# Optimization experiments

Measured on AMD Instinct MI355X. Metric: run time of the kernel, lower is better.

## Reference

```python
import jax, jax.numpy as jnp
import numpy as np

EPS = 1e-5

def conv_block(x, w, b, a, g, bt):
    # x: [B,Cin,T,F]; w: [Cout,Cin]; b: [Cout]; a: scalar PReLU slope; g,bt: [Cout,F]
    y = jnp.einsum('bctf,oc->botf', x, w) + b[None, :, None, None]
    y = jnp.maximum(y, 0.0) + a * jnp.minimum(y, 0.0)  # PReLU (single shared slope)
    mu = jnp.mean(y, axis=(1, 3), keepdims=True)
    var = jnp.var(y, axis=(1, 3), keepdims=True)       # unbiased=False
    y = (y - mu) / jnp.sqrt(var + EPS)
    return y * g[None, :, None, :] + bt[None, :, None, :]

# vmap over heads: weights have leading head axis, x is shared
_head_block = jax.vmap(conv_block, in_axes=(None, 0, 0, 0, 0, 0))


def setup_inputs() -> dict:
    key = jax.random.key(0)
    B, C, T, F = 8, 64, 1024, 64
    H, HID = 4, 4
    DV = C // H
    ks = jax.random.split(key, 16)
    s = 1.0 / np.sqrt(C)
    inp = {
        'x': jax.random.normal(ks[0], (B, C, T, F), jnp.float32),
        # per-head Q conv blocks
        'qw': jax.random.normal(ks[1], (H, HID, C), jnp.float32) * s,
        'qb': jax.random.normal(ks[2], (H, HID), jnp.float32) * 0.01,
        'qa': jnp.full((H,), 0.25, jnp.float32),
        'qg': jnp.ones((H, HID, F), jnp.float32),
        'qbeta': jnp.zeros((H, HID, F), jnp.float32),
        # per-head K conv blocks
        'kw': jax.random.normal(ks[3], (H, HID, C), jnp.float32) * s,
        'kb': jax.random.normal(ks[4], (H, HID), jnp.float32) * 0.01,
        'ka': jnp.full((H,), 0.25, jnp.float32),
        'kg': jnp.ones((H, HID, F), jnp.float32),
        'kbeta': jnp.zeros((H, HID, F), jnp.float32),
        # per-head V conv blocks (out = C//H)
        'vw': jax.random.normal(ks[5], (H, DV, C), jnp.float32) * s,
        'vb': jax.random.normal(ks[6], (H, DV), jnp.float32) * 0.01,
        'va': jnp.full((H,), 0.25, jnp.float32),
        'vg': jnp.ones((H, DV, F), jnp.float32),
        'vbeta': jnp.zeros((H, DV, F), jnp.float32),
        # final 'likear' conv block
        'lw': jax.random.normal(ks[7], (C, C), jnp.float32) * s,
        'lb': jax.random.normal(ks[8], (C,), jnp.float32) * 0.01,
        'la': jnp.float32(0.25),
        'lg': jnp.ones((C, F), jnp.float32),
        'lbeta': jnp.zeros((C, F), jnp.float32),
    }
    return inp


def reference(x, qw, qb, qa, qg, qbeta, kw, kb, ka, kg, kbeta,
              vw, vb, va, vg, vbeta, lw, lb, la, lg, lbeta):
    B, C, T, F = x.shape
    H = qw.shape[0]
    HID = qw.shape[1]
    DV = C // H
    embed = H * F  # embed_size = num_heads * num_freqs

    Q = _head_block(x, qw, qb, qa, qg, qbeta)  # [H,B,HID,T,F]
    K = _head_block(x, kw, kb, ka, kg, kbeta)  # [H,B,HID,T,F]
    V = _head_block(x, vw, vb, va, vg, vbeta)  # [H,B,DV,T,F]

    # cat over dim 0 == head-major reshape; transpose(1,2)+flatten(2)
    Ql = Q.reshape(H * B, HID, T, F).transpose(0, 2, 1, 3).reshape(H * B, T, HID * F)
    Kl = K.reshape(H * B, HID, T, F).transpose(0, 2, 1, 3).reshape(H * B, T, HID * F)
    Vl = V.reshape(H * B, DV, T, F).transpose(0, 2, 1, 3).reshape(H * B, T, DV * F)

    scores = jnp.einsum('ntd,nsd->nts', Ql, Kl) / jnp.sqrt(jnp.float32(embed))
    attn = jax.nn.softmax(scores, axis=-1)               # [HB,T,T]
    A = jnp.einsum('nts,nsd->ntd', attn, Vl)             # [HB,T,DV*F]

    A = A.reshape(H * B, T, DV, F).transpose(0, 2, 1, 3)  # [HB,DV,T,F]
    A = A.reshape(H, B, DV, T, F).transpose(1, 0, 2, 3, 4).reshape(B, C, T, F)

    out = conv_block(A, lw, lb, la, lg, lbeta)
    return out + x
```

## Files before the change

kernel.cpp:

```cpp
#include <hip/hip_runtime.h>

typedef unsigned short u16;
typedef unsigned int u32;
typedef __attribute__((ext_vector_type(8))) short short8;
typedef __attribute__((ext_vector_type(4))) float f32x4;

#define EPSV 1e-5f

__device__ __forceinline__ u16 f2bf(float f) {
    unsigned u = __float_as_uint(f);
    u += 0x7fffu + ((u >> 16) & 1u);
    return (u16)(u >> 16);
}

__device__ __forceinline__ f32x4 mfma_bf16(short8 a, short8 b, f32x4 c) {
    return __builtin_amdgcn_mfma_f32_16x16x32_bf16(a, b, c, 0, 0, 0);
}

__device__ __forceinline__ void gload_lds16(const void* g, void* l) {
    __builtin_amdgcn_global_load_lds((const __attribute__((address_space(1))) void*)g,
                                     (__attribute__((address_space(3))) void*)l, 16, 0, 0);
}

__device__ __forceinline__ u32 packgb(float g, float bt) {
    return (u32)f2bf(g) | ((u32)f2bf(bt) << 16);
}

__global__ __launch_bounds__(256) void k_prep_qkv(
    const float* __restrict__ qw, const float* __restrict__ kw, const float* __restrict__ vw,
    u16* __restrict__ wq)
{
    const int tid = threadIdx.x;
#pragma unroll
    for (int i = 0; i < 24; i++) {
        int idx = tid + i * 256;
        int row = idx >> 6;
        float wv = (row < 16) ? qw[idx] : ((row < 32) ? kw[idx - 1024] : vw[idx - 2048]);
        wq[idx] = f2bf(wv);
    }
}

__global__ __launch_bounds__(256) void k_prep_l(
    const float* __restrict__ lw, const float* __restrict__ lg, const float* __restrict__ lbt,
    u16* __restrict__ lwb, u32* __restrict__ lgb)
{
    const int tid = threadIdx.x;
#pragma unroll
    for (int i = 0; i < 16; i++) {
        int idx = tid + i * 256;
        lwb[idx] = f2bf(lw[idx]);
        lgb[idx] = packgb(lg[idx], lbt[idx]);
    }
}

__global__ __launch_bounds__(512) void k_qkv(
    const float* __restrict__ x, const u16* __restrict__ wq,
    const float* __restrict__ qb, const float* __restrict__ qa,
    const float* __restrict__ qg, const float* __restrict__ qbt,
    const float* __restrict__ kb, const float* __restrict__ ka,
    const float* __restrict__ kg, const float* __restrict__ kbt,
    const float* __restrict__ vb, const float* __restrict__ va,
    const float* __restrict__ vg, const float* __restrict__ vbt,
    u16* __restrict__ Qb, u16* __restrict__ Kb, u16* __restrict__ Vb)
{
    __shared__ u16 xT[64][66];
    __shared__ float ys[96][66];
    __shared__ float bias_s[96], slope_s[96];

    const int tid = threadIdx.x, w = tid >> 6, lane = tid & 63;
    const int b = blockIdx.x >> 10, t = blockIdx.x & 1023;
    const int lc = lane & 15, grp = lane >> 4;

    if (tid < 96) {
        int row = tid; float bv, sv;
        if (row < 16)      { bv = qb[row];      sv = qa[row >> 2]; }
        else if (row < 32) { bv = kb[row - 16]; sv = ka[(row - 16) >> 2]; }
        else               { bv = vb[row - 32]; sv = va[(row - 32) >> 4]; }
        bias_s[row] = bv; slope_s[row] = sv;
    }
    const float* xbt = x + ((size_t)(b * 64) * 1024 + t) * 64;
#pragma unroll
    for (int k = 0; k < 2; k++) {
        int chunk = tid + k * 512;
        int c = chunk >> 4, q = chunk & 15;
        float4 v = *(const float4*)(xbt + (size_t)c * 65536 + q * 4);
        xT[q * 4 + 0][c] = f2bf(v.x);
        xT[q * 4 + 1][c] = f2bf(v.y);
        xT[q * 4 + 2][c] = f2bf(v.z);
        xT[q * 4 + 3][c] = f2bf(v.w);
    }
    __syncthreads();

#pragma unroll
    for (int i = 0; i < 3; i++) {
        int tile = w * 3 + i;
        int mt = tile >> 2, nt = tile & 3;
        f32x4 acc = {0.f, 0.f, 0.f, 0.f};
#pragma unroll
        for (int kt = 0; kt < 2; kt++) {
            short8 a  = *(const short8*)(wq + (mt * 16 + lc) * 64 + kt * 32 + grp * 8);
            short8 bf = *(const short8*)(&xT[nt * 16 + lc][kt * 32 + grp * 8]);
            acc = mfma_bf16(a, bf, acc);
        }
        int colf = nt * 16 + lc;
#pragma unroll
        for (int j = 0; j < 4; j++) {
            int row = mt * 16 + grp * 4 + j;
            float y = acc[j] + bias_s[row];
            float sl = slope_s[row];
            y = (y > 0.f) ? y : sl * y;
            ys[row][colf] = y;
        }
    }
    __syncthreads();

    if (w < 4) {
        const int h = w;
        float v0[16]; float s = 0.f, ss = 0.f;
#pragma unroll
        for (int o = 0; o < 16; o++) { float y = ys[32 + h * 16 + o][lane]; v0[o] = y; s += y; ss += y * y; }
#pragma unroll
        for (int m = 1; m < 64; m <<= 1) { s += __shfl_xor(s, m, 64); ss += __shfl_xor(ss, m, 64); }
        float mu = s * (1.f / 1024.f), var = ss * (1.f / 1024.f) - mu * mu;
        float rs = rsqrtf(var + EPSV);
        size_t base = ((size_t)(h * 8 + b) * 1024 + t) * 1024;
#pragma unroll
        for (int o = 0; o < 16; o++) {
            float val = (v0[o] - mu) * rs * vg[(h * 16 + o) * 64 + lane] + vbt[(h * 16 + o) * 64 + lane];
            Vb[base + o * 64 + lane] = f2bf(val);
        }
    } else {
        const int h = w - 4;
        {
            float v0[4]; float s = 0.f, ss = 0.f;
#pragma unroll
            for (int o = 0; o < 4; o++) { float y = ys[h * 4 + o][lane]; v0[o] = y; s += y; ss += y * y; }
#pragma unroll
            for (int m = 1; m < 64; m <<= 1) { s += __shfl_xor(s, m, 64); ss += __shfl_xor(ss, m, 64); }
            float mu = s * (1.f / 256.f), var = ss * (1.f / 256.f) - mu * mu;
            float rs = rsqrtf(var + EPSV);
            size_t base = ((size_t)(h * 8 + b) * 1024 + t) * 256;
#pragma unroll
            for (int o = 0; o < 4; o++) {
                float val = (v0[o] - mu) * rs * qg[(h * 4 + o) * 64 + lane] + qbt[(h * 4 + o) * 64 + lane];
                Qb[base + o * 64 + lane] = f2bf(val);
            }
        }
        {
            float v0[4]; float s = 0.f, ss = 0.f;
#pragma unroll
            for (int o = 0; o < 4; o++) { float y = ys[16 + h * 4 + o][lane]; v0[o] = y; s += y; ss += y * y; }
#pragma unroll
            for (int m = 1; m < 64; m <<= 1) { s += __shfl_xor(s, m, 64); ss += __shfl_xor(ss, m, 64); }
            float mu = s * (1.f / 256.f), var = ss * (1.f / 256.f) - mu * mu;
            float rs = rsqrtf(var + EPSV);
            size_t base = ((size_t)(h * 8 + b) * 1024 + t) * 256;
#pragma unroll
            for (int o = 0; o < 4; o++) {
                float val = (v0[o] - mu) * rs * kg[(h * 4 + o) * 64 + lane] + kbt[(h * 4 + o) * 64 + lane];
                Kb[base + o * 64 + lane] = f2bf(val);
            }
        }
    }
}

__global__ __launch_bounds__(256) void k_vtrans(const u16* __restrict__ Vb, u16* __restrict__ Vt)
{
    __shared__ u16 ts[64][72];
    const int tid = threadIdx.x;
    const int idx = blockIdx.x;
    const int n = idx >> 8, rest = idx & 255;
    const int s0 = (rest >> 4) * 64, d0 = (rest & 15) * 64;
    const size_t nb = (size_t)n << 20;

#pragma unroll
    for (int i = 0; i < 2; i++) {
        int chunk = tid + i * 256;
        int row = chunk >> 3, q = chunk & 7;
        uint4 v = *(const uint4*)(Vb + nb + (size_t)(s0 + row) * 1024 + d0 + q * 8);
        *(uint4*)(&ts[row][q * 8]) = v;
    }
    __syncthreads();
#pragma unroll
    for (int i = 0; i < 2; i++) {
        int chunk = tid + i * 256;
        int orow = chunk >> 3, q = chunk & 7;
        uint4 o;
        o.x = (unsigned)ts[q * 8 + 0][orow] | ((unsigned)ts[q * 8 + 1][orow] << 16);
        o.y = (unsigned)ts[q * 8 + 2][orow] | ((unsigned)ts[q * 8 + 3][orow] << 16);
        o.z = (unsigned)ts[q * 8 + 4][orow] | ((unsigned)ts[q * 8 + 5][orow] << 16);
        o.w = (unsigned)ts[q * 8 + 6][orow] | ((unsigned)ts[q * 8 + 7][orow] << 16);
        *(uint4*)(Vt + nb + (size_t)(d0 + orow) * 1024 + s0 + q * 8) = o;
    }
}

__global__ __launch_bounds__(256) void k_attn(const u16* __restrict__ Qb, const u16* __restrict__ Kb,
                                              u16* __restrict__ P)
{
    __shared__ u16 Ks[4][16 * 256];
    __shared__ float red[2][4][16];

    const int bid = blockIdx.x;
    const int n = (bid & 7) + ((bid >> 9) << 3);
    const int qt = (bid >> 3) & 63;
    const int q0 = qt * 16;
    const int tid = threadIdx.x, w = tid >> 6, lane = tid & 63;
    const int grp = lane >> 4, lc = lane & 15;

    const u16* Qn = Qb + ((size_t)n << 18);
    const u16* Kn = Kb + ((size_t)n << 18);

    short8 qf[8];
#pragma unroll
    for (int kt = 0; kt < 8; kt++)
        qf[kt] = *(const short8*)(Qn + (size_t)(q0 + lc) * 256 + kt * 32 + grp * 8);

    u16* KsW = Ks[w];
    const int l_row = lane >> 5;
    const int l_cs = (lane & 31) * 8;

    f32x4 sacc[16];
#pragma unroll
    for (int st = 0; st < 16; st++) {
        int s0 = w * 256 + st * 16;
#pragma unroll
        for (int c = 0; c < 8; c++) {
            int row = c * 2 + l_row;
            int col = l_cs ^ ((row & 7) << 3);
            gload_lds16(Kn + (size_t)(s0 + row) * 256 + col, KsW + c * 512);
        }
        __syncthreads();
        f32x4 a = {0.f, 0.f, 0.f, 0.f};
#pragma unroll
        for (int kt = 0; kt < 8; kt++) {
            int off = lc * 256 + ((kt * 32 + grp * 8) ^ ((lc & 7) << 3));
            short8 kf = *(const short8*)(KsW + off);
            a = mfma_bf16(qf[kt], kf, a);
        }
        sacc[st] = a;
        __syncthreads();
    }

    float mx[4] = {-1e30f, -1e30f, -1e30f, -1e30f};
#pragma unroll
    for (int st = 0; st < 16; st++)
#pragma unroll
        for (int j = 0; j < 4; j++) {
            float v = sacc[st][j] * 0.0625f;
            sacc[st][j] = v;
            mx[j] = fmaxf(mx[j], v);
        }
#pragma unroll
    for (int m = 1; m < 16; m <<= 1)
#pragma unroll
        for (int j = 0; j < 4; j++) mx[j] = fmaxf(mx[j], __shfl_xor(mx[j], m, 64));

    if (lc == 0) {
#pragma unroll
        for (int j = 0; j < 4; j++) red[0][w][grp * 4 + j] = mx[j];
    }
    __syncthreads();
    float gm[4], sm[4] = {0.f, 0.f, 0.f, 0.f};
#pragma unroll
    for (int j = 0; j < 4; j++) {
        int row = grp * 4 + j;
        gm[j] = fmaxf(fmaxf(red[0][0][row], red[0][1][row]), fmaxf(red[0][2][row], red[0][3][row]));
    }
#pragma unroll
    for (int st = 0; st < 16; st++)
#pragma unroll
        for (int j = 0; j < 4; j++) {
            float p = __expf(sacc[st][j] - gm[j]);
            sacc[st][j] = p;
            sm[j] += p;
        }
#pragma unroll
    for (int m = 1; m < 16; m <<= 1)
#pragma unroll
        for (int j = 0; j < 4; j++) sm[j] += __shfl_xor(sm[j], m, 64);
    if (lc == 0) {
#pragma unroll
        for (int j = 0; j < 4; j++) red[1][w][grp * 4 + j] = sm[j];
    }
    __syncthreads();

    u16* Pn = P + ((size_t)n << 20);
    float inv[4];
#pragma unroll
    for (int j = 0; j < 4; j++) {
        int row = grp * 4 + j;
        float tot = red[1][0][row] + red[1][1][row] + red[1][2][row] + red[1][3][row];
        inv[j] = 1.f / tot;
    }
#pragma unroll
    for (int st = 0; st < 16; st++)
#pragma unroll
        for (int j = 0; j < 4; j++) {
            Pn[(size_t)(q0 + grp * 4 + j) * 1024 + w * 256 + st * 16 + lc] = f2bf(sacc[st][j] * inv[j]);
        }
}

__global__ __launch_bounds__(512, 1) void k_pv(const u16* __restrict__ P, const u16* __restrict__ Vt,
                                               float* __restrict__ outf, u16* __restrict__ outb,
                                               int use_bf16)
{
    __shared__ u16 lds[3][4][128 * 32];

    const int bid = blockIdx.x;
    const int n = (bid & 7) + ((bid >> 7) << 3);
    const int tile = (bid >> 3) & 15;
    const int tm = tile >> 2, tn = tile & 3;
    const int tid = threadIdx.x, w = tid >> 6, lane = tid & 63;
    const int wr = w >> 2, wc = w & 3;
    const int lc = lane & 15, grp = lane >> 4;

    const u16* Pa = P  + ((size_t)n << 20) + (size_t)tm * 256 * 1024;
    const u16* Va = Vt + ((size_t)n << 20) + (size_t)tn * 256 * 1024;

    const int srow = tid >> 2, scc = tid & 3;
    const int scol = (scc ^ (srow & 3)) * 8;
    const int ldst = w * 512;

    f32x4 acc[8][4];
#pragma unroll
    for (int mi = 0; mi < 8; mi++)
#pragma unroll
        for (int ni = 0; ni < 4; ni++) acc[mi][ni] = (f32x4){0.f, 0.f, 0.f, 0.f};

#define STAGE_PV(ks_, pb_)                                                        \
    {                                                                             \
        size_t k0_ = (size_t)(ks_) * 32;                                          \
        gload_lds16(Pa + (size_t)srow * 1024 + k0_ + scol,         &lds[pb_][0][ldst]); \
        gload_lds16(Pa + (size_t)(128 + srow) * 1024 + k0_ + scol, &lds[pb_][1][ldst]); \
        gload_lds16(Va + (size_t)srow * 1024 + k0_ + scol,         &lds[pb_][2][ldst]); \
        gload_lds16(Va + (size_t)(128 + srow) * 1024 + k0_ + scol, &lds[pb_][3][ldst]); \
    }

    STAGE_PV(0, 0);
    STAGE_PV(1, 1);
    asm volatile("s_waitcnt vmcnt(4)" ::: "memory");
    __builtin_amdgcn_s_barrier();

    const int rxor = (lc & 3);
    int cur = 0;
    for (int ks = 0; ks < 32; ks++) {
        int nxt = cur + 2; if (nxt >= 3) nxt -= 3;
        if (ks < 30) STAGE_PV(ks + 2, nxt);

        const u16* As = lds[cur][wr];
        const u16* Bs = lds[cur][2 + (wc >> 1)];
        const int brow0 = (wc & 1) * 64;

        short8 af[8], bf[4];
#pragma unroll
        for (int mi = 0; mi < 8; mi++)
            af[mi] = *(const short8*)(As + (mi * 16 + lc) * 32 + ((grp ^ rxor) * 8));
#pragma unroll
        for (int ni = 0; ni < 4; ni++)
            bf[ni] = *(const short8*)(Bs + (brow0 + ni * 16 + lc) * 32 + ((grp ^ rxor) * 8));

        __builtin_amdgcn_s_setprio(1);
#pragma unroll
        for (int mi = 0; mi < 8; mi++)
#pragma unroll
            for (int ni = 0; ni < 4; ni++)
                acc[mi][ni] = mfma_bf16(af[mi], bf[ni], acc[mi][ni]);
        __builtin_amdgcn_s_setprio(0);

        if (ks < 31) {
            if (ks < 30) {
                asm volatile("s_waitcnt vmcnt(4) lgkmcnt(0)" ::: "memory");
            } else {
                asm volatile("s_waitcnt vmcnt(0) lgkmcnt(0)" ::: "memory");
            }
            __builtin_amdgcn_s_barrier();
        }
        cur = (cur == 2) ? 0 : cur + 1;
    }
#undef STAGE_PV

    const int h = n >> 3, b = n & 7;
    if (use_bf16) {
#pragma unroll
        for (int mi = 0; mi < 8; mi++)
#pragma unroll
            for (int ni = 0; ni < 4; ni++) {
                int d = tn * 256 + wc * 64 + ni * 16 + lc;
                int c = h * 16 + (d >> 6), f = d & 63;
#pragma unroll
                for (int j = 0; j < 4; j++) {
                    int trow = tm * 256 + wr * 128 + mi * 16 + grp * 4 + j;
                    outb[(((size_t)b * 64 + c) * 1024 + trow) * 64 + f] = f2bf(acc[mi][ni][j]);
                }
            }
    } else {
#pragma unroll
        for (int mi = 0; mi < 8; mi++)
#pragma unroll
            for (int ni = 0; ni < 4; ni++) {
                int d = tn * 256 + wc * 64 + ni * 16 + lc;
                int c = h * 16 + (d >> 6), f = d & 63;
#pragma unroll
                for (int j = 0; j < 4; j++) {
                    int trow = tm * 256 + wr * 128 + mi * 16 + grp * 4 + j;
                    outf[(((size_t)b * 64 + c) * 1024 + trow) * 64 + f] = acc[mi][ni][j];
                }
            }
    }
}

__global__ __launch_bounds__(256, 2) void k_final(
    const float* __restrict__ Af, const u16* __restrict__ Ab, const float* __restrict__ x,
    const u16* __restrict__ lwbf, const u32* __restrict__ lgb,
    const float* __restrict__ lbias, const float* __restrict__ la,
    float* __restrict__ out, int use_bf16)
{
    __shared__ u16 AT[256][66];
    __shared__ u32 gb_s[64][66];
    __shared__ float bias_s[64];

    const int tid = threadIdx.x, w = tid >> 6, lane = tid & 63;
    const int b = blockIdx.x >> 8, tb = blockIdx.x & 255;
    const int t0 = tb * 4, t = t0 + w;
    const int lc = lane & 15, grp = lane >> 4;

    if (tid < 64) bias_s[tid] = lbias[tid];
#pragma unroll
    for (int i = 0; i < 16; i++) {
        int idx = tid + i * 256;
        gb_s[idx >> 6][idx & 63] = lgb[idx];
    }
    if (use_bf16) {
#pragma unroll
        for (int k = 0; k < 8; k++) {
            int idx = k * 256 + tid;
            int q = idx & 7, c = (idx >> 3) & 63, tl = idx >> 9;
            uint4 v = *(const uint4*)(Ab + ((size_t)(b * 64 + c) * 1024 + t0 + tl) * 64 + q * 8);
            const u16* pv = (const u16*)&v;
            int n = tl * 64 + q * 8;
#pragma unroll
            for (int i = 0; i < 8; i++) AT[n + i][c] = pv[i];
        }
    } else {
#pragma unroll
        for (int k = 0; k < 16; k++) {
            int idx = k * 256 + tid;
            int q = idx & 15, c = (idx >> 4) & 63, tl = idx >> 10;
            float4 v = *(const float4*)(Af + ((size_t)(b * 64 + c) * 1024 + t0 + tl) * 64 + q * 4);
            int n = tl * 64 + q * 4;
            AT[n + 0][c] = f2bf(v.x);
            AT[n + 1][c] = f2bf(v.y);
            AT[n + 2][c] = f2bf(v.z);
            AT[n + 3][c] = f2bf(v.w);
        }
    }
    __syncthreads();

    short8 bfr[4][2];
#pragma unroll
    for (int nt = 0; nt < 4; nt++)
#pragma unroll
        for (int kt = 0; kt < 2; kt++)
            bfr[nt][kt] = *(const short8*)(&AT[w * 64 + nt * 16 + lc][kt * 32 + grp * 8]);

    f32x4 acc[4][4];
#pragma unroll
    for (int mt = 0; mt < 4; mt++) {
        short8 af[2];
#pragma unroll
        for (int kt = 0; kt < 2; kt++)
            af[kt] = *(const short8*)(lwbf + (mt * 16 + lc) * 64 + kt * 32 + grp * 8);
#pragma unroll
        for (int nt = 0; nt < 4; nt++) {
            f32x4 a = {0.f, 0.f, 0.f, 0.f};
            a = mfma_bf16(af[0], bfr[nt][0], a);
            a = mfma_bf16(af[1], bfr[nt][1], a);
            acc[mt][nt] = a;
        }
    }

    const float slope = la[0];
    float s = 0.f, ss = 0.f;
#pragma unroll
    for (int mt = 0; mt < 4; mt++)
#pragma unroll
        for (int nt = 0; nt < 4; nt++)
#pragma unroll
            for (int j = 0; j < 4; j++) {
                float y = acc[mt][nt][j] + bias_s[mt * 16 + grp * 4 + j];
                y = (y > 0.f) ? y : slope * y;
                acc[mt][nt][j] = y;
                s += y; ss += y * y;
            }
#pragma unroll
    for (int m = 1; m < 64; m <<= 1) { s += __shfl_xor(s, m, 64); ss += __shfl_xor(ss, m, 64); }
    float mu = s * (1.f / 4096.f), var = ss * (1.f / 4096.f) - mu * mu;
    float rs = rsqrtf(var + EPSV);

#pragma unroll
    for (int mt = 0; mt < 4; mt++)
#pragma unroll
        for (int nt = 0; nt < 4; nt++)
#pragma unroll
            for (int j = 0; j < 4; j++) {
                int row = mt * 16 + grp * 4 + j, f = nt * 16 + lc;
                u32 p = gb_s[row][f];
                float g = __uint_as_float(p << 16), bt = __uint_as_float(p & 0xffff0000u);
                size_t gi = ((size_t)(b * 64 + row) * 1024 + t) * 64 + f;
                out[gi] = (acc[mt][nt][j] - mu) * rs * g + bt + x[gi];
            }
}

extern "C" void kernel_launch(void* const* d_in, const int* in_sizes, int n_in,
                              void* d_out, int out_size, void* d_ws, size_t ws_size,
                              hipStream_t stream)
{
    const float* x    = (const float*)d_in[0];
    const float* qw   = (const float*)d_in[1];
    const float* qb   = (const float*)d_in[2];
    const float* qa   = (const float*)d_in[3];
    const float* qg   = (const float*)d_in[4];
    const float* qbt  = (const float*)d_in[5];
    const float* kw   = (const float*)d_in[6];
    const float* kb   = (const float*)d_in[7];
    const float* ka   = (const float*)d_in[8];
    const float* kg   = (const float*)d_in[9];
    const float* kbt  = (const float*)d_in[10];
    const float* vw   = (const float*)d_in[11];
    const float* vb   = (const float*)d_in[12];
    const float* va   = (const float*)d_in[13];
    const float* vg   = (const float*)d_in[14];
    const float* vbt  = (const float*)d_in[15];
    const float* lw   = (const float*)d_in[16];
    const float* lb   = (const float*)d_in[17];
    const float* la   = (const float*)d_in[18];
    const float* lg   = (const float*)d_in[19];
    const float* lbt  = (const float*)d_in[20];

    float* out = (float*)d_out;

    u16* Vb = (u16*)d_ws;
    u16* Vt = (u16*)((char*)d_ws + ((size_t)64 << 20));
    u16* P  = Vb;
    u16* Qb = (u16*)d_out;
    u16* Kb = (u16*)((char*)d_out + ((size_t)16 << 20));

    u16* wqkv = Vt;
    u16* lwb  = (u16*)d_ws;
    u32* lgb  = (u32*)((char*)d_ws + 8192);

    const int use_bf16 = (ws_size >= ((size_t)192 << 20)) ? 1 : 0;
    u16* Ab = (u16*)((char*)d_ws + ((size_t)128 << 20));

    k_prep_qkv<<<dim3(1), dim3(256), 0, stream>>>(qw, kw, vw, wqkv);
    k_qkv<<<dim3(8192), dim3(512), 0, stream>>>(x, wqkv, qb, qa, qg, qbt,
                                                kb, ka, kg, kbt,
                                                vb, va, vg, vbt, Qb, Kb, Vb);
    k_vtrans<<<dim3(8192), dim3(256), 0, stream>>>(Vb, Vt);
    k_attn<<<dim3(2048), dim3(256), 0, stream>>>(Qb, Kb, P);
    k_pv<<<dim3(512), dim3(512), 0, stream>>>(P, Vt, out, Ab, use_bf16);
    k_prep_l<<<dim3(1), dim3(256), 0, stream>>>(lw, lg, lbt, lwb, lgb);
    k_final<<<dim3(2048), dim3(256), 0, stream>>>(out, Ab, x, lwb, lgb, lb, la, out, use_bf16);
}
```

Measured before the change: 325.1 us.

## Keep QKV conv outputs in registers and normalize per warp without LDS staging

The QKV projection kernel now assigns one 16-row output tile per warp (6 warps, 384 threads) and keeps the MFMA accumulators in registers. Each warp computes the per-head layer-norm statistics with intra-wave shuffles instead of writing results to a shared ys buffer and resynchronizing. This removes the 96x66 float LDS array and the second barrier, and lowers shared memory use so more blocks can be resident. In exchange, the output stores now follow the MFMA fragment layout, which is less contiguous than the old one-row-per-lane writes, and the block has fewer threads to load x.

```diff
diff --git a/kernel.cpp b/kernel.cpp
--- a/kernel.cpp
+++ b/kernel.cpp
@@ -53,7 +53,7 @@
     }
 }
 
-__global__ __launch_bounds__(512) void k_qkv(
+__global__ __launch_bounds__(384) void k_qkv(
     const float* __restrict__ x, const u16* __restrict__ wq,
     const float* __restrict__ qb, const float* __restrict__ qa,
     const float* __restrict__ qg, const float* __restrict__ qbt,
@@ -64,7 +64,6 @@
     u16* __restrict__ Qb, u16* __restrict__ Kb, u16* __restrict__ Vb)
 {
     __shared__ u16 xT[64][66];
-    __shared__ float ys[96][66];
     __shared__ float bias_s[96], slope_s[96];
 
     const int tid = threadIdx.x, w = tid >> 6, lane = tid & 63;
@@ -79,9 +78,7 @@
         bias_s[row] = bv; slope_s[row] = sv;
     }
     const float* xbt = x + ((size_t)(b * 64) * 1024 + t) * 64;
-#pragma unroll
-    for (int k = 0; k < 2; k++) {
-        int chunk = tid + k * 512;
+    for (int chunk = tid; chunk < 1024; chunk += 384) {
         int c = chunk >> 4, q = chunk & 15;
         float4 v = *(const float4*)(xbt + (size_t)c * 65536 + q * 4);
         xT[q * 4 + 0][c] = f2bf(v.x);
@@ -91,76 +88,87 @@
     }
     __syncthreads();
 
-#pragma unroll
-    for (int i = 0; i < 3; i++) {
-        int tile = w * 3 + i;
-        int mt = tile >> 2, nt = tile & 3;
-        f32x4 acc = {0.f, 0.f, 0.f, 0.f};
-#pragma unroll
-        for (int kt = 0; kt < 2; kt++) {
-            short8 a  = *(const short8*)(wq + (mt * 16 + lc) * 64 + kt * 32 + grp * 8);
-            short8 bf = *(const short8*)(&xT[nt * 16 + lc][kt * 32 + grp * 8]);
-            acc = mfma_bf16(a, bf, acc);
-        }
-        int colf = nt * 16 + lc;
+    short8 af[2];
+#pragma unroll
+    for (int kt = 0; kt < 2; kt++)
+        af[kt] = *(const short8*)(wq + (w * 16 + lc) * 64 + kt * 32 + grp * 8);
+
+    f32x4 acc[4];
+#pragma unroll
+    for (int nt = 0; nt < 4; nt++) {
+        f32x4 a = {0.f, 0.f, 0.f, 0.f};
+        a = mfma_bf16(af[0], *(const short8*)(&xT[nt * 16 + lc][0 * 32 + grp * 8]), a);
+        a = mfma_bf16(af[1], *(const short8*)(&xT[nt * 16 + lc][1 * 32 + grp * 8]), a);
+        acc[nt] = a;
+    }
+
+#pragma unroll
+    for (int nt = 0; nt < 4; nt++)
 #pragma unroll
         for (int j = 0; j < 4; j++) {
-            int row = mt * 16 + grp * 4 + j;
-            float y = acc[j] + bias_s[row];
-            float sl = slope_s[row];
-            y = (y > 0.f) ? y : sl * y;
-            ys[row][colf] = y;
-        }
-    }
-    __syncthreads();
-
-    if (w < 4) {
-        const int h = w;
-        float v0[16]; float s = 0.f, ss = 0.f;
-#pragma unroll
-        for (int o = 0; o < 16; o++) { float y = ys[32 + h * 16 + o][lane]; v0[o] = y; s += y; ss += y * y; }
+            int row = w * 16 + grp * 4 + j;
+            float y = acc[nt][j] + bias_s[row];
+            acc[nt][j] = (y > 0.f) ? y : slope_s[row] * y;
+        }
+
+    if (w == 0) {
+        float s = 0.f, ss = 0.f;
+#pragma unroll
+        for (int nt = 0; nt < 4; nt++)
+#pragma unroll
+            for (int j = 0; j < 4; j++) { float y = acc[nt][j]; s += y; ss += y * y; }
+#pragma unroll
+        for (int m = 1; m < 16; m <<= 1) { s += __shfl_xor(s, m, 64); ss += __shfl_xor(ss, m, 64); }
+        float mu = s * (1.f / 256.f), var = ss * (1.f / 256.f) - mu * mu;
+        float rs = rsqrtf(var + EPSV);
+        size_t base = ((size_t)(grp * 8 + b) * 1024 + t) * 256;
+#pragma unroll
+        for (int nt = 0; nt < 4; nt++)
+#pragma unroll
+            for (int j = 0; j < 4; j++) {
+                int gi = (grp * 4 + j) * 64 + nt * 16 + lc;
+                float val = (acc[nt][j] - mu) * rs * qg[gi] + qbt[gi];
+                Qb[base + j * 64 + nt * 16 + lc] = f2bf(val);
+            }
+    } else if (w == 1) {
+        float s = 0.f, ss = 0.f;
+#pragma unroll
+        for (int nt = 0; nt < 4; nt++)
+#pragma unroll
+            for (int j = 0; j < 4; j++) { float y = acc[nt][j]; s += y; ss += y * y; }
+#pragma unroll
+        for (int m = 1; m < 16; m <<= 1) { s += __shfl_xor(s, m, 64); ss += __shfl_xor(ss, m, 64); }
+        float mu = s * (1.f / 256.f), var = ss * (1.f / 256.f) - mu * mu;
+        float rs = rsqrtf(var + EPSV);
+        size_t base = ((size_t)(grp * 8 + b) * 1024 + t) * 256;
+#pragma unroll
+        for (int nt = 0; nt < 4; nt++)
+#pragma unroll
+            for (int j = 0; j < 4; j++) {
+                int gi = (grp * 4 + j) * 64 + nt * 16 + lc;
+                float val = (acc[nt][j] - mu) * rs * kg[gi] + kbt[gi];
+                Kb[base + j * 64 + nt * 16 + lc] = f2bf(val);
+            }
+    } else {
+        const int hv = w - 2;
+        float s = 0.f, ss = 0.f;
+#pragma unroll
+        for (int nt = 0; nt < 4; nt++)
+#pragma unroll
+            for (int j = 0; j < 4; j++) { float y = acc[nt][j]; s += y; ss += y * y; }
 #pragma unroll
         for (int m = 1; m < 64; m <<= 1) { s += __shfl_xor(s, m, 64); ss += __shfl_xor(ss, m, 64); }
         float mu = s * (1.f / 1024.f), var = ss * (1.f / 1024.f) - mu * mu;
         float rs = rsqrtf(var + EPSV);
-        size_t base = ((size_t)(h * 8 + b) * 1024 + t) * 1024;
-#pragma unroll
-        for (int o = 0; o < 16; o++) {
-            float val = (v0[o] - mu) * rs * vg[(h * 16 + o) * 64 + lane] + vbt[(h * 16 + o) * 64 + lane];
-            Vb[base + o * 64 + lane] = f2bf(val);
-        }
-    } else {
-        const int h = w - 4;
-        {
-            float v0[4]; float s = 0.f, ss = 0.f;
-#pragma unroll
-            for (int o = 0; o < 4; o++) { float y = ys[h * 4 + o][lane]; v0[o] = y; s += y; ss += y * y; }
-#pragma unroll
-            for (int m = 1; m < 64; m <<= 1) { s += __shfl_xor(s, m, 64); ss += __shfl_xor(ss, m, 64); }
-            float mu = s * (1.f / 256.f), var = ss * (1.f / 256.f) - mu * mu;
-            float rs = rsqrtf(var + EPSV);
-            size_t base = ((size_t)(h * 8 + b) * 1024 + t) * 256;
-#pragma unroll
-            for (int o = 0; o < 4; o++) {
-                float val = (v0[o] - mu) * rs * qg[(h * 4 + o) * 64 + lane] + qbt[(h * 4 + o) * 64 + lane];
-                Qb[base + o * 64 + lane] = f2bf(val);
-            }
-        }
-        {
-            float v0[4]; float s = 0.f, ss = 0.f;
-#pragma unroll
-            for (int o = 0; o < 4; o++) { float y = ys[16 + h * 4 + o][lane]; v0[o] = y; s += y; ss += y * y; }
-#pragma unroll
-            for (int m = 1; m < 64; m <<= 1) { s += __shfl_xor(s, m, 64); ss += __shfl_xor(ss, m, 64); }
-            float mu = s * (1.f / 256.f), var = ss * (1.f / 256.f) - mu * mu;
-            float rs = rsqrtf(var + EPSV);
-            size_t base = ((size_t)(h * 8 + b) * 1024 + t) * 256;
-#pragma unroll
-            for (int o = 0; o < 4; o++) {
-                float val = (v0[o] - mu) * rs * kg[(h * 4 + o) * 64 + lane] + kbt[(h * 4 + o) * 64 + lane];
-                Kb[base + o * 64 + lane] = f2bf(val);
-            }
-        }
+        size_t base = ((size_t)(hv * 8 + b) * 1024 + t) * 1024;
+#pragma unroll
+        for (int nt = 0; nt < 4; nt++)
+#pragma unroll
+            for (int j = 0; j < 4; j++) {
+                int gi = (hv * 16 + grp * 4 + j) * 64 + nt * 16 + lc;
+                float val = (acc[nt][j] - mu) * rs * vg[gi] + vbt[gi];
+                Vb[base + (grp * 4 + j) * 64 + nt * 16 + lc] = f2bf(val);
+            }
     }
 }
 
@@ -553,7 +561,7 @@
     u16* Ab = (u16*)((char*)d_ws + ((size_t)128 << 20));
 
     k_prep_qkv<<<dim3(1), dim3(256), 0, stream>>>(qw, kw, vw, wqkv);
-    k_qkv<<<dim3(8192), dim3(512), 0, stream>>>(x, wqkv, qb, qa, qg, qbt,
+    k_qkv<<<dim3(8192), dim3(384), 0, stream>>>(x, wqkv, qb, qa, qg, qbt,
                                                 kb, ka, kg, kbt,
                                                 vb, va, vg, vbt, Qb, Kb, Vb);
     k_vtrans<<<dim3(8192), dim3(256), 0, stream>>>(Vb, Vt);
```

New measurement: 319.8 us, median of 3. No clear change (-1.6%).
